# Kernel optimization log

Measured on AMD Instinct MI355X. Metric: run time of the kernel, lower is better.

## Reference

```python
import jax, jax.numpy as jnp
import numpy as np

B, N, E = 32, 1024, 512   # docs, word-nodes per doc, hyperedges per doc
V = 50001                 # n_node + 1 (padding idx 0)
D = 300                   # initialFeatureSize == n_hid
H = 300                   # hiddenSize (output of gat2)
NEG = -9e15


def _leaky(v, alpha):
    return jnp.where(v > 0, v, alpha * v)


def _hypergat_layer(x, adj, w, w2, w3, a, a2, wc, alpha, concat):
    # x: [B,N,Fin], adj: [B,E,N] 0/1 incidence. Eval mode: dropout = identity.
    Fo = w2.shape[1]
    x4 = x @ w2                                   # [B,N,Fo]
    if w is not None:                             # transfer=True branch
        x = x @ w                                 # [B,N,Fo]
    mask = adj > 0                                # [B,E,N]
    # edge attention: score per node, constant word-context query
    s1 = _leaky(wc @ a[:Fo, 0] + x4 @ a[Fo:, 0], alpha)          # [B,N]
    att_edge = jax.nn.softmax(jnp.where(mask, s1[:, None, :], NEG), axis=2)  # [B,E,N]
    edge = att_edge @ x                           # [B,E,Fo] hyperedge features
    edge4 = edge @ w3                             # [B,E,Fo]
    # node attention: score(node n, edge e) = leaky(x4[n]@a2_top + edge4[e]@a2_bot)
    sc = _leaky((x4 @ a2[:Fo, 0])[:, None, :] + (edge4 @ a2[Fo:, 0])[:, :, None], alpha)  # [B,E,N]
    att_node = jax.nn.softmax(jnp.where(mask, sc, NEG).transpose(0, 2, 1), axis=2)        # [B,N,E]
    node = att_node @ edge                        # [B,N,Fo]
    return jax.nn.elu(node) if concat else node


def setup_inputs() -> dict:
    key = jax.random.key(0)
    ks = jax.random.split(key, 16)
    stdv = 1.0 / np.sqrt(H)  # DocumentGraph.reset_parameters uniform_(-stdv, stdv) on all params
    u = lambda k, shape: jax.random.uniform(k, shape, jnp.float32, -stdv, stdv)
    return dict(
        inputs=jax.random.randint(ks[0], (B, N), 0, V),
        HT=(jax.random.uniform(ks[1], (B, E, N)) < 0.10).astype(jnp.int32),
        emb=u(ks[2], (V, D)),
        w2_1=u(ks[3], (D, D)), w3_1=u(ks[4], (D, D)),
        a_1=u(ks[5], (2 * D, 1)), a2_1=u(ks[6], (2 * D, 1)), wc_1=u(ks[7], (D,)),
        w_2=u(ks[8], (D, H)), w2_2=u(ks[9], (D, H)), w3_2=u(ks[10], (H, H)),
        a_2=u(ks[11], (2 * H, 1)), a2_2=u(ks[12], (2 * H, 1)), wc_2=u(ks[13], (H,)),
    )


def reference(inputs, HT, emb, w2_1, w3_1, a_1, a2_1, wc_1,
              w_2, w2_2, w3_2, a_2, a2_2, wc_2):
    x = emb[inputs]                                # [B,N,D] embedding lookup
    # gat1: transfer=False, concat=True, alpha=0.1
    x = _hypergat_layer(x, HT, None, w2_1, w3_1, a_1, a2_1, wc_1, 0.1, True)
    # gat2: transfer=True, bias=False, concat=False, alpha=0.2
    x = _hypergat_layer(x, HT, w_2, w2_2, w3_2, a_2, a2_2, wc_2, 0.2, False)
    return x
```

## Files before the change

kernel.cpp:

```cpp
#include <hip/hip_runtime.h>
#include <hip/hip_bf16.h>

#define CB 32
#define CN 1024
#define CE 512
#define CD 300
#define EP 320
#define UCAP 320

__global__ void k_embed(const int* __restrict__ idx, const float* __restrict__ emb,
                        float* __restrict__ X) {
    int gid = blockIdx.x * blockDim.x + threadIdx.x;
    const int total = CB * CN * 75;
    if (gid >= total) return;
    int r = gid / 75, c = gid % 75;
    int e = idx[r];
    reinterpret_cast<float4*>(X)[(size_t)r * 75 + c] =
        reinterpret_cast<const float4*>(emb)[(size_t)e * 75 + c];
}

__global__ void k_ebits(const int* __restrict__ HT, unsigned long long* __restrict__ ebits) {
    int gw = (blockIdx.x * blockDim.x + threadIdx.x) >> 6;
    int lane = threadIdx.x & 63;
    const int* hrow = HT + (size_t)gw * CN;
#pragma unroll
    for (int c = 0; c < 16; ++c) {
        unsigned long long bal = __ballot(hrow[(c << 6) + lane] != 0);
        if (lane == 0) ebits[(size_t)gw * 16 + c] = bal;
    }
}

__global__ __launch_bounds__(512) void k_bitT(const unsigned long long* __restrict__ ebits,
        unsigned long long* __restrict__ nbits) {
    __shared__ unsigned long long w[8][64];
    int b = blockIdx.x >> 4, nc = blockIdx.x & 15;
    int tid = threadIdx.x, ec = tid >> 6, lane = tid & 63;
    w[ec][lane] = ebits[((size_t)b * CE + (ec << 6) + lane) * 16 + nc];
    __syncthreads();
    unsigned long long out = 0;
#pragma unroll
    for (int j = 0; j < 64; ++j)
        out |= ((w[ec][j] >> lane) & 1ull) << j;
    nbits[((size_t)b * CN + (nc << 6) + lane) * 8 + ec] = out;
}

__global__ void k_prep(const float* __restrict__ w2_1, const float* __restrict__ w3_1,
                       const float* __restrict__ a_1, const float* __restrict__ a2_1,
                       const float* __restrict__ w2_2, const float* __restrict__ w3_2,
                       const float* __restrict__ a_2, const float* __restrict__ a2_2,
                       float* __restrict__ vecs) {
    int which = blockIdx.x;
    int t = threadIdx.x;
    if (t >= CD) return;
    const float* W; const float* v;
    switch (which) {
        case 0:  W = w2_1; v = a_1 + CD;  break;
        case 1:  W = w2_1; v = a2_1;      break;
        case 2:  W = w3_1; v = a2_1 + CD; break;
        case 3:  W = w2_2; v = a_2 + CD;  break;
        case 4:  W = w2_2; v = a2_2;      break;
        default: W = w3_2; v = a2_2 + CD; break;
    }
    float s = 0.f;
    for (int j = 0; j < CD; ++j) s += W[(size_t)t * CD + j] * v[j];
    vecs[which * CD + t] = s;
}

__global__ __launch_bounds__(256) void k_gemm300(const float* __restrict__ A,
                                                 const float* __restrict__ W,
                                                 float* __restrict__ C, int M,
                                                 int lda, int ldc) {
    __shared__ float As[64][20];
    __shared__ float Ws[16][68];
    int tid = threadIdx.x;
    int n0 = blockIdx.x * 64, m0 = blockIdx.y * 64;
    int tx = tid & 15, ty = tid >> 4;
    int la_r = tid >> 2, la_c = (tid & 3) << 2;
    int lw_r = tid >> 4, lw_c = (tid & 15) << 2;
    float acc[4][4] = {};
    for (int k0 = 0; k0 < CD; k0 += 16) {
        {
            int kc = k0 + la_c;
            const float* Ap = A + (size_t)(m0 + la_r) * lda + kc;
            float4 av;
            if (kc + 3 < CD) av = *reinterpret_cast<const float4*>(Ap);
            else {
                av.x = kc     < CD ? Ap[0] : 0.f;
                av.y = kc + 1 < CD ? Ap[1] : 0.f;
                av.z = kc + 2 < CD ? Ap[2] : 0.f;
                av.w = 0.f;
            }
            *reinterpret_cast<float4*>(&As[la_r][la_c]) = av;
        }
        {
            int kr = k0 + lw_r;
            float4 wv = {0.f, 0.f, 0.f, 0.f};
            if (kr < CD) {
                const float* Wp = W + (size_t)kr * CD + n0 + lw_c;
                if (n0 + lw_c + 3 < CD) wv = *reinterpret_cast<const float4*>(Wp);
                else {
                    if (n0 + lw_c     < CD) wv.x = Wp[0];
                    if (n0 + lw_c + 1 < CD) wv.y = Wp[1];
                    if (n0 + lw_c + 2 < CD) wv.z = Wp[2];
                }
            }
            *reinterpret_cast<float4*>(&Ws[lw_r][lw_c]) = wv;
        }
        __syncthreads();
#pragma unroll
        for (int k = 0; k < 16; ++k) {
            float av[4];
#pragma unroll
            for (int i = 0; i < 4; ++i) av[i] = As[ty * 4 + i][k];
            float4 bv = *reinterpret_cast<const float4*>(&Ws[k][tx * 4]);
            float bb[4] = {bv.x, bv.y, bv.z, bv.w};
#pragma unroll
            for (int i = 0; i < 4; ++i)
#pragma unroll
                for (int j = 0; j < 4; ++j) acc[i][j] += av[i] * bb[j];
        }
        __syncthreads();
    }
    for (int i = 0; i < 4; ++i) {
        int m = m0 + ty * 4 + i;
        int n = n0 + tx * 4;
        float* Cp = C + (size_t)m * ldc + n;
        if (n + 3 < CD) {
            float4 v = {acc[i][0], acc[i][1], acc[i][2], acc[i][3]};
            *reinterpret_cast<float4*>(Cp) = v;
        } else {
            for (int j = 0; j < 4; ++j) if (n + j < CD) Cp[j] = acc[i][j];
        }
    }
}

__global__ void k_score(const float* __restrict__ X, const float* __restrict__ av,
                        const float* __restrict__ pv, const float* __restrict__ wc,
                        const float* __restrict__ a_orig,
                        float alpha, float* __restrict__ s1, float* __restrict__ p, int M) {
    int gw = (blockIdx.x * blockDim.x + threadIdx.x) >> 6;
    int lane = threadIdx.x & 63;
    if (gw >= M) return;
    const float* row = X + (size_t)gw * CD;
    float d1 = 0.f, d2 = 0.f, dc = 0.f;
    for (int d = lane; d < CD; d += 64) {
        float x = row[d];
        d1 += x * av[d];
        d2 += x * pv[d];
        dc += wc[d] * a_orig[d];
    }
    for (int o = 32; o; o >>= 1) {
        d1 += __shfl_down(d1, o);
        d2 += __shfl_down(d2, o);
        dc += __shfl_down(dc, o);
    }
    if (lane == 0) {
        float v = dc + d1;
        s1[gw] = v > 0.f ? v : alpha * v;
        p[gw] = d2;
    }
}

__global__ __launch_bounds__(1024) void k_bmax(const float* __restrict__ s1,
                                               float* __restrict__ e1) {
    __shared__ float red[16];
    int b = blockIdx.x, t = threadIdx.x;
    float v = s1[b * CN + t];
    float m = v;
    for (int o = 32; o; o >>= 1) m = fmaxf(m, __shfl_xor(m, o));
    if ((t & 63) == 0) red[t >> 6] = m;
    __syncthreads();
    if (t == 0) {
        float mm = red[0];
        for (int i = 1; i < 16; ++i) mm = fmaxf(mm, red[i]);
        red[0] = mm;
    }
    __syncthreads();
    e1[b * CN + t] = __expf(v - red[0]);
}

__global__ __launch_bounds__(256) void k_edge_agg(const unsigned long long* __restrict__ ebits,
        const float* __restrict__ e1, const float* __restrict__ Xs,
        const float* __restrict__ qvec, float* __restrict__ edge, float* __restrict__ q) {
    int gw = (blockIdx.x * blockDim.x + threadIdx.x) >> 6;
    int lane = threadIdx.x & 63;
    int b = gw >> 9;
    const unsigned long long* eb = ebits + (size_t)gw * 16;
    const float* e1b = e1 + b * CN;
    const float4* Xb4 = reinterpret_cast<const float4*>(Xs + (size_t)b * CN * CD);
    float4 a0 = {0.f, 0.f, 0.f, 0.f}, a1 = {0.f, 0.f, 0.f, 0.f};
    float den = 0.f;
    bool tail = lane < 11;
    int any = 0;
#pragma unroll
    for (int c = 0; c < 16; ++c) {
        int n0 = c << 6;
        float wv = e1b[n0 + lane];
        unsigned long long bal = eb[c];
        any |= (bal != 0ull);
        while (bal) {
            int j0 = (int)__ffsll(bal) - 1; bal &= bal - 1ull;
            float w0 = __shfl(wv, j0);
            const float4* r0 = Xb4 + (size_t)(n0 + j0) * 75;
            if (bal) {
                int j1 = (int)__ffsll(bal) - 1; bal &= bal - 1ull;
                float w1 = __shfl(wv, j1);
                const float4* r1 = Xb4 + (size_t)(n0 + j1) * 75;
                float4 v0a = r0[lane];
                float4 v1a = r1[lane];
                float4 v0b, v1b;
                if (tail) { v0b = r0[64 + lane]; v1b = r1[64 + lane]; }
                den += w0; den += w1;
                a0.x += w0 * v0a.x; a0.y += w0 * v0a.y; a0.z += w0 * v0a.z; a0.w += w0 * v0a.w;
                a0.x += w1 * v1a.x; a0.y += w1 * v1a.y; a0.z += w1 * v1a.z; a0.w += w1 * v1a.w;
                if (tail) {
                    a1.x += w0 * v0b.x; a1.y += w0 * v0b.y; a1.z += w0 * v0b.z; a1.w += w0 * v0b.w;
                    a1.x += w1 * v1b.x; a1.y += w1 * v1b.y; a1.z += w1 * v1b.z; a1.w += w1 * v1b.w;
                }
            } else {
                float4 v0a = r0[lane];
                float4 v0b;
                if (tail) v0b = r0[64 + lane];
                den += w0;
                a0.x += w0 * v0a.x; a0.y += w0 * v0a.y; a0.z += w0 * v0a.z; a0.w += w0 * v0a.w;
                if (tail) {
                    a1.x += w0 * v0b.x; a1.y += w0 * v0b.y; a1.z += w0 * v0b.z; a1.w += w0 * v0b.w;
                }
            }
        }
    }
    float inv = any ? 1.f / den : 0.f;
    float4 o0 = {a0.x * inv, a0.y * inv, a0.z * inv, a0.w * inv};
    float4 o1 = {a1.x * inv, a1.y * inv, a1.z * inv, a1.w * inv};
    float4* er4 = reinterpret_cast<float4*>(edge + (size_t)gw * EP);
    er4[lane] = o0;
    if (tail) er4[64 + lane] = o1;
    else if (lane < 16) er4[64 + lane] = make_float4(0.f, 0.f, 0.f, 0.f);
    const float4* qv4 = reinterpret_cast<const float4*>(qvec);
    float4 qa = qv4[lane];
    float d2 = o0.x * qa.x + o0.y * qa.y + o0.z * qa.z + o0.w * qa.w;
    if (tail) {
        float4 qb2 = qv4[64 + lane];
        d2 += o1.x * qb2.x + o1.y * qb2.y + o1.z * qb2.z + o1.w * qb2.w;
    }
    for (int o = 32; o; o >>= 1) d2 += __shfl_down(d2, o);
    if (lane == 0) q[gw] = d2;
}

#define ACC16(vv, ww) do { \
    acc[0][0] += (ww).x * (vv).x; acc[0][1] += (ww).x * (vv).y; \
    acc[0][2] += (ww).x * (vv).z; acc[0][3] += (ww).x * (vv).w; \
    acc[1][0] += (ww).y * (vv).x; acc[1][1] += (ww).y * (vv).y; \
    acc[1][2] += (ww).y * (vv).z; acc[1][3] += (ww).y * (vv).w; \
    acc[2][0] += (ww).z * (vv).x; acc[2][1] += (ww).z * (vv).y; \
    acc[2][2] += (ww).z * (vv).z; acc[2][3] += (ww).z * (vv).w; \
    acc[3][0] += (ww).w * (vv).x; acc[3][1] += (ww).w * (vv).y; \
    acc[3][2] += (ww).w * (vv).z; acc[3][3] += (ww).w * (vv).w; \
} while (0)

__global__ __launch_bounds__(320, 8) void k_node_attn(const unsigned long long* __restrict__ nbits,
        const float* __restrict__ p, const float* __restrict__ q,
        const float* __restrict__ edge, float alpha, int do_elu, float* __restrict__ out) {
    __shared__ float4 wsc[4][UCAP];
    __shared__ __align__(8) unsigned short ul[4][UCAP];
    __shared__ int ucnt_s[4], flag_s[4];
    __shared__ float gpn[16], gmx[16], gsc[16];
    __shared__ int gct[16];
    int blk = blockIdx.x;
    int b = blk >> 6, n0 = (blk & 63) << 4;
    int tid = threadIdx.x, wv = tid >> 6, lane = tid & 63;
    const float* qb = q + b * CE;

    if (wv < 4) {
        float pn[4]; const unsigned long long* nb[4];
#pragma unroll
        for (int k = 0; k < 4; ++k) {
            int n = n0 + 4 * wv + k;
            pn[k] = p[b * CN + n];
            nb[k] = nbits + ((size_t)b * CN + n) * 8;
        }
        float sc[4][8];
        int cnt[4] = {0, 0, 0, 0};
        float mx[4] = {-3.4e38f, -3.4e38f, -3.4e38f, -3.4e38f};
        int ubits = 0;
#pragma unroll
        for (int j = 0; j < 8; ++j) {
            int e = lane + (j << 6);
            float qe = qb[e];
            int many = 0;
#pragma unroll
            for (int k = 0; k < 4; ++k) {
                int m = (int)((nb[k][j] >> lane) & 1ull);
                float v = pn[k] + qe;
                v = v > 0.f ? v : alpha * v;
                v = m ? v : -3.0e38f;
                cnt[k] += m; many |= m;
                mx[k] = fmaxf(mx[k], v);
                sc[k][j] = v;
            }
            ubits |= (many ? 1 : 0) << j;
        }
#pragma unroll
        for (int k = 0; k < 4; ++k) {
            for (int o = 32; o; o >>= 1) {
                mx[k] = fmaxf(mx[k], __shfl_xor(mx[k], o));
                cnt[k] += __shfl_xor(cnt[k], o);
            }
        }
        float scale[4];
#pragma unroll
        for (int k = 0; k < 4; ++k) {
            float s = 0.f;
#pragma unroll
            for (int j = 0; j < 8; ++j) { float w8 = __expf(sc[k][j] - mx[k]); sc[k][j] = w8; s += w8; }
            for (int o = 32; o; o >>= 1) s += __shfl_xor(s, o);
            scale[k] = cnt[k] > 0 ? 1.f / s : 1.f;
        }
        int base = 0;
        unsigned long long lmask = (1ull << lane) - 1ull;
#pragma unroll
        for (int j = 0; j < 8; ++j) {
            unsigned long long bal = __ballot((ubits >> j) & 1);
            if ((ubits >> j) & 1) {
                int off = base + (int)__popcll(bal & lmask);
                if (off < UCAP) {
                    ul[wv][off] = (unsigned short)(lane + (j << 6));
                    wsc[wv][off] = make_float4(sc[0][j] * scale[0], sc[1][j] * scale[1],
                                               sc[2][j] * scale[2], sc[3][j] * scale[3]);
                }
            }
            base += (int)__popcll(bal);
        }
        if (lane == 0) {
            ucnt_s[wv] = base < UCAP ? base : UCAP;
            flag_s[wv] = (cnt[0] == 0) | (cnt[1] == 0) | (cnt[2] == 0) | (cnt[3] == 0) |
                         (base > UCAP);
            gpn[wv*4+0]=pn[0]; gmx[wv*4+0]=mx[0]; gsc[wv*4+0]=scale[0]; gct[wv*4+0]=cnt[0];
            gpn[wv*4+1]=pn[1]; gmx[wv*4+1]=mx[1]; gsc[wv*4+1]=scale[1]; gct[wv*4+1]=cnt[1];
            gpn[wv*4+2]=pn[2]; gmx[wv*4+2]=mx[2]; gsc[wv*4+2]=scale[2]; gct[wv*4+2]=cnt[2];
            gpn[wv*4+3]=pn[3]; gmx[wv*4+3]=mx[3]; gsc[wv*4+3]=scale[3]; gct[wv*4+3]=cnt[3];
        }
    }
    __syncthreads();

    int grp = tid / 80;
    int j4 = tid - grp * 80;
    const float4* eb4 = reinterpret_cast<const float4*>(edge + (size_t)b * CE * EP) + j4;
    int cnt = ucnt_s[grp], bad = flag_s[grp];
    float acc[4][4] = {};
    if (!bad) {
        int i = 0;
        for (; i + 4 <= cnt; i += 4) {
            ushort4 uu = *reinterpret_cast<const ushort4*>(&ul[grp][i]);
            float4 w0 = wsc[grp][i],     w1 = wsc[grp][i + 1];
            float4 w2 = wsc[grp][i + 2], w3 = wsc[grp][i + 3];
            float4 v0 = eb4[(size_t)uu.x * 80], v1 = eb4[(size_t)uu.y * 80];
            float4 v2 = eb4[(size_t)uu.z * 80], v3 = eb4[(size_t)uu.w * 80];
            ACC16(v0, w0); ACC16(v1, w1); ACC16(v2, w2); ACC16(v3, w3);
        }
        for (; i < cnt; ++i) {
            int e = ul[grp][i];
            float4 v = eb4[(size_t)e * 80];
            float4 w = wsc[grp][i];
            ACC16(v, w);
        }
    } else {
        float pnk[4], mxk[4], sck[4]; int ctk[4];
        const unsigned long long* nbr[4];
#pragma unroll
        for (int k = 0; k < 4; ++k) {
            pnk[k] = gpn[grp*4+k]; mxk[k] = gmx[grp*4+k]; sck[k] = gsc[grp*4+k]; ctk[k] = gct[grp*4+k];
            nbr[k] = nbits + ((size_t)b * CN + n0 + grp * 4 + k) * 8;
        }
        for (int e = 0; e < CE; ++e) {
            float4 v = eb4[(size_t)e * 80];
            float qe = qb[e];
#pragma unroll
            for (int k = 0; k < 4; ++k) {
                int m = (int)((nbr[k][e >> 6] >> (e & 63)) & 1ull);
                float vv = pnk[k] + qe; vv = vv > 0.f ? vv : alpha * vv;
                float w = ctk[k] == 0 ? (1.f / CE) : (m ? __expf(vv - mxk[k]) * sck[k] : 0.f);
                acc[k][0] += w * v.x; acc[k][1] += w * v.y; acc[k][2] += w * v.z; acc[k][3] += w * v.w;
            }
        }
    }
    if (j4 < 75) {
#pragma unroll
        for (int ni = 0; ni < 4; ++ni) {
            float4 o = {acc[ni][0], acc[ni][1], acc[ni][2], acc[ni][3]};
            if (do_elu) {
                o.x = o.x > 0.f ? o.x : expm1f(o.x);
                o.y = o.y > 0.f ? o.y : expm1f(o.y);
                o.z = o.z > 0.f ? o.z : expm1f(o.z);
                o.w = o.w > 0.f ? o.w : expm1f(o.w);
            }
            *reinterpret_cast<float4*>(out + ((size_t)b * CN + n0 + grp * 4 + ni) * CD + j4 * 4) = o;
        }
    }
}

extern "C" void kernel_launch(void* const* d_in, const int* in_sizes, int n_in,
                              void* d_out, int out_size, void* d_ws, size_t ws_size,
                              hipStream_t stream) {
    const int*   inputs = (const int*)d_in[0];
    const int*   HT     = (const int*)d_in[1];
    const float* emb    = (const float*)d_in[2];
    const float* w2_1   = (const float*)d_in[3];
    const float* w3_1   = (const float*)d_in[4];
    const float* a_1    = (const float*)d_in[5];
    const float* a2_1   = (const float*)d_in[6];
    const float* wc_1   = (const float*)d_in[7];
    const float* w_2    = (const float*)d_in[8];
    const float* w2_2   = (const float*)d_in[9];
    const float* w3_2   = (const float*)d_in[10];
    const float* a_2    = (const float*)d_in[11];
    const float* a2_2   = (const float*)d_in[12];
    const float* wc_2   = (const float*)d_in[13];

    char* ws = (char*)d_ws;
    float* big0               = (float*)(ws);
    float* big1               = (float*)(ws + 39321600);
    float* edge               = (float*)(ws + 78643200);
    unsigned long long* ebits = (unsigned long long*)(ws + 99614720);
    unsigned long long* nbits = (unsigned long long*)(ws + 101711872);
    float* s1                 = (float*)(ws + 103809024);
    float* p                  = (float*)(ws + 103940096);
    float* e1                 = (float*)(ws + 104071168);
    float* qv                 = (float*)(ws + 104202240);
    float* vecs               = (float*)(ws + 104267776);

    k_embed<<<9600, 256, 0, stream>>>(inputs, emb, big0);
    k_ebits<<<4096, 256, 0, stream>>>(HT, ebits);
    k_bitT<<<512, 512, 0, stream>>>(ebits, nbits);
    k_prep<<<6, 320, 0, stream>>>(w2_1, w3_1, a_1, a2_1, w2_2, w3_2, a_2, a2_2, vecs);

    k_score<<<CB * CN / 4, 256, 0, stream>>>(big0, vecs, vecs + CD, wc_1, a_1, 0.1f, s1, p, CB * CN);
    k_bmax<<<CB, 1024, 0, stream>>>(s1, e1);
    k_edge_agg<<<4096, 256, 0, stream>>>(ebits, e1, big0, vecs + 2 * CD, edge, qv);
    k_node_attn<<<2048, 320, 0, stream>>>(nbits, p, qv, edge, 0.1f, 1, big0);

    k_score<<<CB * CN / 4, 256, 0, stream>>>(big0, vecs + 3 * CD, vecs + 4 * CD, wc_2, a_2, 0.2f, s1, p, CB * CN);
    k_gemm300<<<dim3(5, 512), 256, 0, stream>>>(big0, w_2, big1, CB * CN, CD, CD);
    k_bmax<<<CB, 1024, 0, stream>>>(s1, e1);
    k_edge_agg<<<4096, 256, 0, stream>>>(ebits, e1, big1, vecs + 5 * CD, edge, qv);
    k_node_attn<<<2048, 320, 0, stream>>>(nbits, p, qv, edge, 0.2f, 0, (float*)d_out);
}
```

Baseline: 735.4 us.

## Precompute hyperedge member lists and gather scalar rows in edge aggregation

Adds a kernel that turns each hyperedge's bitmask into a compact ushort list of member nodes plus a degree. Edge aggregation walks that list four members at a time with scalar loads, and falls back to the bitmask path if a degree exceeds the cap. The aim is to drop the per-bit ffs/shuffle overhead and get more loads in flight. Node attention now unrolls its gather to eight edges and drops the min-blocks launch bound. The cost is an extra kernel, extra workspace, and scalar rather than float4 loads.

```diff
diff --git a/kernel.cpp b/kernel.cpp
--- a/kernel.cpp
+++ b/kernel.cpp
@@ -7,6 +7,7 @@
 #define CD 300
 #define EP 320
 #define UCAP 320
+#define MCAP 192
 
 __global__ void k_embed(const int* __restrict__ idx, const float* __restrict__ emb,
                         float* __restrict__ X) {
@@ -42,6 +43,26 @@
     for (int j = 0; j < 64; ++j)
         out |= ((w[ec][j] >> lane) & 1ull) << j;
     nbits[((size_t)b * CN + (nc << 6) + lane) * 8 + ec] = out;
+}
+
+__global__ void k_members(const unsigned long long* __restrict__ ebits,
+                          unsigned short* __restrict__ mem, int* __restrict__ degs) {
+    int gw = (blockIdx.x * blockDim.x + threadIdx.x) >> 6;
+    int lane = threadIdx.x & 63;
+    const unsigned long long* eb = ebits + (size_t)gw * 16;
+    unsigned short* lst = mem + (size_t)gw * MCAP;
+    int base = 0;
+    unsigned long long lmask = (1ull << lane) - 1ull;
+#pragma unroll
+    for (int c = 0; c < 16; ++c) {
+        unsigned long long w = eb[c];
+        if ((w >> lane) & 1ull) {
+            int off = base + (int)__popcll(w & lmask);
+            if (off < MCAP) lst[off] = (unsigned short)((c << 6) + lane);
+        }
+        base += (int)__popcll(w);
+    }
+    if (lane == 0) degs[gw] = base;
 }
 
 __global__ void k_prep(const float* __restrict__ w2_1, const float* __restrict__ w3_1,
@@ -179,70 +200,88 @@
     e1[b * CN + t] = __expf(v - red[0]);
 }
 
-__global__ __launch_bounds__(256) void k_edge_agg(const unsigned long long* __restrict__ ebits,
+__global__ __launch_bounds__(256) void k_edge_agg(const unsigned short* __restrict__ mem,
+        const int* __restrict__ degs, const unsigned long long* __restrict__ ebits,
         const float* __restrict__ e1, const float* __restrict__ Xs,
         const float* __restrict__ qvec, float* __restrict__ edge, float* __restrict__ q) {
     int gw = (blockIdx.x * blockDim.x + threadIdx.x) >> 6;
     int lane = threadIdx.x & 63;
     int b = gw >> 9;
-    const unsigned long long* eb = ebits + (size_t)gw * 16;
     const float* e1b = e1 + b * CN;
-    const float4* Xb4 = reinterpret_cast<const float4*>(Xs + (size_t)b * CN * CD);
-    float4 a0 = {0.f, 0.f, 0.f, 0.f}, a1 = {0.f, 0.f, 0.f, 0.f};
+    const float* Xb = Xs + (size_t)b * CN * CD;
+    int deg = degs[gw];
+    float a0 = 0.f, a1 = 0.f, a2 = 0.f, a3 = 0.f, a4 = 0.f;
     float den = 0.f;
-    bool tail = lane < 11;
-    int any = 0;
-#pragma unroll
-    for (int c = 0; c < 16; ++c) {
-        int n0 = c << 6;
-        float wv = e1b[n0 + lane];
-        unsigned long long bal = eb[c];
-        any |= (bal != 0ull);
-        while (bal) {
-            int j0 = (int)__ffsll(bal) - 1; bal &= bal - 1ull;
-            float w0 = __shfl(wv, j0);
-            const float4* r0 = Xb4 + (size_t)(n0 + j0) * 75;
-            if (bal) {
-                int j1 = (int)__ffsll(bal) - 1; bal &= bal - 1ull;
-                float w1 = __shfl(wv, j1);
-                const float4* r1 = Xb4 + (size_t)(n0 + j1) * 75;
-                float4 v0a = r0[lane];
-                float4 v1a = r1[lane];
-                float4 v0b, v1b;
-                if (tail) { v0b = r0[64 + lane]; v1b = r1[64 + lane]; }
-                den += w0; den += w1;
-                a0.x += w0 * v0a.x; a0.y += w0 * v0a.y; a0.z += w0 * v0a.z; a0.w += w0 * v0a.w;
-                a0.x += w1 * v1a.x; a0.y += w1 * v1a.y; a0.z += w1 * v1a.z; a0.w += w1 * v1a.w;
-                if (tail) {
-                    a1.x += w0 * v0b.x; a1.y += w0 * v0b.y; a1.z += w0 * v0b.z; a1.w += w0 * v0b.w;
-                    a1.x += w1 * v1b.x; a1.y += w1 * v1b.y; a1.z += w1 * v1b.z; a1.w += w1 * v1b.w;
-                }
-            } else {
-                float4 v0a = r0[lane];
-                float4 v0b;
-                if (tail) v0b = r0[64 + lane];
-                den += w0;
-                a0.x += w0 * v0a.x; a0.y += w0 * v0a.y; a0.z += w0 * v0a.z; a0.w += w0 * v0a.w;
-                if (tail) {
-                    a1.x += w0 * v0b.x; a1.y += w0 * v0b.y; a1.z += w0 * v0b.z; a1.w += w0 * v0b.w;
-                }
-            }
-        }
-    }
-    float inv = any ? 1.f / den : 0.f;
-    float4 o0 = {a0.x * inv, a0.y * inv, a0.z * inv, a0.w * inv};
-    float4 o1 = {a1.x * inv, a1.y * inv, a1.z * inv, a1.w * inv};
-    float4* er4 = reinterpret_cast<float4*>(edge + (size_t)gw * EP);
-    er4[lane] = o0;
-    if (tail) er4[64 + lane] = o1;
-    else if (lane < 16) er4[64 + lane] = make_float4(0.f, 0.f, 0.f, 0.f);
-    const float4* qv4 = reinterpret_cast<const float4*>(qvec);
-    float4 qa = qv4[lane];
-    float d2 = o0.x * qa.x + o0.y * qa.y + o0.z * qa.z + o0.w * qa.w;
-    if (tail) {
-        float4 qb2 = qv4[64 + lane];
-        d2 += o1.x * qb2.x + o1.y * qb2.y + o1.z * qb2.z + o1.w * qb2.w;
-    }
+    bool tail = lane < (CD - 256);
+    if (deg <= MCAP) {
+        const unsigned short* lst = mem + (size_t)gw * MCAP;
+        int i = 0;
+        for (; i + 4 <= deg; i += 4) {
+            ushort4 nn = *reinterpret_cast<const ushort4*>(lst + i);
+            float w0 = e1b[nn.x], w1 = e1b[nn.y], w2 = e1b[nn.z], w3 = e1b[nn.w];
+            const float* r0 = Xb + (size_t)nn.x * CD;
+            const float* r1 = Xb + (size_t)nn.y * CD;
+            const float* r2 = Xb + (size_t)nn.z * CD;
+            const float* r3 = Xb + (size_t)nn.w * CD;
+            float v00 = r0[lane], v01 = r0[lane + 64], v02 = r0[lane + 128], v03 = r0[lane + 192];
+            float v10 = r1[lane], v11 = r1[lane + 64], v12 = r1[lane + 128], v13 = r1[lane + 192];
+            float v20 = r2[lane], v21 = r2[lane + 64], v22 = r2[lane + 128], v23 = r2[lane + 192];
+            float v30 = r3[lane], v31 = r3[lane + 64], v32 = r3[lane + 128], v33 = r3[lane + 192];
+            float v04 = 0.f, v14 = 0.f, v24 = 0.f, v34 = 0.f;
+            if (tail) { v04 = r0[lane + 256]; v14 = r1[lane + 256]; v24 = r2[lane + 256]; v34 = r3[lane + 256]; }
+            den += w0; den += w1; den += w2; den += w3;
+            a0 += w0 * v00; a0 += w1 * v10; a0 += w2 * v20; a0 += w3 * v30;
+            a1 += w0 * v01; a1 += w1 * v11; a1 += w2 * v21; a1 += w3 * v31;
+            a2 += w0 * v02; a2 += w1 * v12; a2 += w2 * v22; a2 += w3 * v32;
+            a3 += w0 * v03; a3 += w1 * v13; a3 += w2 * v23; a3 += w3 * v33;
+            a4 += w0 * v04; a4 += w1 * v14; a4 += w2 * v24; a4 += w3 * v34;
+        }
+        for (; i < deg; ++i) {
+            int n = lst[i];
+            float w = e1b[n];
+            const float* r = Xb + (size_t)n * CD;
+            den += w;
+            a0 += w * r[lane];
+            a1 += w * r[lane + 64];
+            a2 += w * r[lane + 128];
+            a3 += w * r[lane + 192];
+            if (tail) a4 += w * r[lane + 256];
+        }
+    } else {
+        const unsigned long long* eb = ebits + (size_t)gw * 16;
+#pragma unroll
+        for (int c = 0; c < 16; ++c) {
+            int n0 = c << 6;
+            float wv = e1b[n0 + lane];
+            unsigned long long bal = eb[c];
+            while (bal) {
+                int jj = (int)__ffsll(bal) - 1;
+                bal &= bal - 1ull;
+                float w = __shfl(wv, jj);
+                const float* row = Xb + (size_t)(n0 + jj) * CD;
+                den += w;
+                a0 += w * row[lane];
+                a1 += w * row[lane + 64];
+                a2 += w * row[lane + 128];
+                a3 += w * row[lane + 192];
+                if (tail) a4 += w * row[lane + 256];
+            }
+        }
+    }
+    float inv = deg > 0 ? 1.f / den : 0.f;
+    float o0 = a0 * inv, o1 = a1 * inv, o2 = a2 * inv, o3 = a3 * inv;
+    float o4 = tail ? a4 * inv : 0.f;
+    float* erow = edge + (size_t)gw * EP;
+    erow[lane]       = o0;
+    erow[lane + 64]  = o1;
+    erow[lane + 128] = o2;
+    erow[lane + 192] = o3;
+    erow[lane + 256] = o4;
+    float d2 = o0 * qvec[lane];
+    d2 += o1 * qvec[lane + 64];
+    d2 += o2 * qvec[lane + 128];
+    d2 += o3 * qvec[lane + 192];
+    if (tail) d2 += o4 * qvec[lane + 256];
     for (int o = 32; o; o >>= 1) d2 += __shfl_down(d2, o);
     if (lane == 0) q[gw] = d2;
 }
@@ -258,7 +297,7 @@
     acc[3][2] += (ww).w * (vv).z; acc[3][3] += (ww).w * (vv).w; \
 } while (0)
 
-__global__ __launch_bounds__(320, 8) void k_node_attn(const unsigned long long* __restrict__ nbits,
+__global__ __launch_bounds__(320) void k_node_attn(const unsigned long long* __restrict__ nbits,
         const float* __restrict__ p, const float* __restrict__ q,
         const float* __restrict__ edge, float alpha, int do_elu, float* __restrict__ out) {
     __shared__ float4 wsc[4][UCAP];
@@ -350,13 +389,21 @@
     float acc[4][4] = {};
     if (!bad) {
         int i = 0;
-        for (; i + 4 <= cnt; i += 4) {
-            ushort4 uu = *reinterpret_cast<const ushort4*>(&ul[grp][i]);
-            float4 w0 = wsc[grp][i],     w1 = wsc[grp][i + 1];
-            float4 w2 = wsc[grp][i + 2], w3 = wsc[grp][i + 3];
-            float4 v0 = eb4[(size_t)uu.x * 80], v1 = eb4[(size_t)uu.y * 80];
-            float4 v2 = eb4[(size_t)uu.z * 80], v3 = eb4[(size_t)uu.w * 80];
-            ACC16(v0, w0); ACC16(v1, w1); ACC16(v2, w2); ACC16(v3, w3);
+        for (; i + 8 <= cnt; i += 8) {
+            ushort4 ua = *reinterpret_cast<const ushort4*>(&ul[grp][i]);
+            ushort4 ub = *reinterpret_cast<const ushort4*>(&ul[grp][i + 4]);
+            float4 v0 = eb4[(size_t)ua.x * 80], v1 = eb4[(size_t)ua.y * 80];
+            float4 v2 = eb4[(size_t)ua.z * 80], v3 = eb4[(size_t)ua.w * 80];
+            float4 v4 = eb4[(size_t)ub.x * 80], v5 = eb4[(size_t)ub.y * 80];
+            float4 v6 = eb4[(size_t)ub.z * 80], v7 = eb4[(size_t)ub.w * 80];
+            { float4 w = wsc[grp][i];     ACC16(v0, w); }
+            { float4 w = wsc[grp][i + 1]; ACC16(v1, w); }
+            { float4 w = wsc[grp][i + 2]; ACC16(v2, w); }
+            { float4 w = wsc[grp][i + 3]; ACC16(v3, w); }
+            { float4 w = wsc[grp][i + 4]; ACC16(v4, w); }
+            { float4 w = wsc[grp][i + 5]; ACC16(v5, w); }
+            { float4 w = wsc[grp][i + 6]; ACC16(v6, w); }
+            { float4 w = wsc[grp][i + 7]; ACC16(v7, w); }
         }
         for (; i < cnt; ++i) {
             int e = ul[grp][i];
@@ -423,25 +470,28 @@
     float* edge               = (float*)(ws + 78643200);
     unsigned long long* ebits = (unsigned long long*)(ws + 99614720);
     unsigned long long* nbits = (unsigned long long*)(ws + 101711872);
-    float* s1                 = (float*)(ws + 103809024);
-    float* p                  = (float*)(ws + 103940096);
-    float* e1                 = (float*)(ws + 104071168);
-    float* qv                 = (float*)(ws + 104202240);
-    float* vecs               = (float*)(ws + 104267776);
+    unsigned short* mem       = (unsigned short*)(ws + 103809024);
+    int* degs                 = (int*)(ws + 110100480);
+    float* s1                 = (float*)(ws + 110166016);
+    float* p                  = (float*)(ws + 110297088);
+    float* e1                 = (float*)(ws + 110428160);
+    float* qv                 = (float*)(ws + 110559232);
+    float* vecs               = (float*)(ws + 110624768);
 
     k_embed<<<9600, 256, 0, stream>>>(inputs, emb, big0);
     k_ebits<<<4096, 256, 0, stream>>>(HT, ebits);
     k_bitT<<<512, 512, 0, stream>>>(ebits, nbits);
+    k_members<<<4096, 256, 0, stream>>>(ebits, mem, degs);
     k_prep<<<6, 320, 0, stream>>>(w2_1, w3_1, a_1, a2_1, w2_2, w3_2, a_2, a2_2, vecs);
 
     k_score<<<CB * CN / 4, 256, 0, stream>>>(big0, vecs, vecs + CD, wc_1, a_1, 0.1f, s1, p, CB * CN);
     k_bmax<<<CB, 1024, 0, stream>>>(s1, e1);
-    k_edge_agg<<<4096, 256, 0, stream>>>(ebits, e1, big0, vecs + 2 * CD, edge, qv);
+    k_edge_agg<<<4096, 256, 0, stream>>>(mem, degs, ebits, e1, big0, vecs + 2 * CD, edge, qv);
     k_node_attn<<<2048, 320, 0, stream>>>(nbits, p, qv, edge, 0.1f, 1, big0);
 
     k_score<<<CB * CN / 4, 256, 0, stream>>>(big0, vecs + 3 * CD, vecs + 4 * CD, wc_2, a_2, 0.2f, s1, p, CB * CN);
     k_gemm300<<<dim3(5, 512), 256, 0, stream>>>(big0, w_2, big1, CB * CN, CD, CD);
     k_bmax<<<CB, 1024, 0, stream>>>(s1, e1);
-    k_edge_agg<<<4096, 256, 0, stream>>>(ebits, e1, big1, vecs + 5 * CD, edge, qv);
+    k_edge_agg<<<4096, 256, 0, stream>>>(mem, degs, ebits, e1, big1, vecs + 5 * CD, edge, qv);
     k_node_attn<<<2048, 320, 0, stream>>>(nbits, p, qv, edge, 0.2f, 0, (float*)d_out);
 }
```

After: 651.7 us. 11.4% less time.
